# Kernel optimization log

Measured on AMD Instinct MI355X. Metric: run time of the kernel, lower is better.

Reference implementation:

```python
import jax, jax.numpy as jnp
import numpy as np

# AFD = permute -> VSSBlock (LN + SS2D Mamba selective scan, residual) -> permute
#       -> x + SAFM(ChannelLayerNorm(x))
C = 64        # in_channels (d_model)
DI = 128      # d_inner = expand(2) * d_model
N = 16        # d_state
R = 4         # dt_rank = ceil(64/16)
K = 4         # scan directions
LN_EPS = 1e-5
CN_EPS = 1e-6
B_, H_, W_ = 8, 64, 64


def setup_inputs() -> dict:
    key = jax.random.key(0)
    ks = jax.random.split(key, 16)
    f = lambda k, s, sc=0.02: jax.random.normal(k, s, jnp.float32) * sc
    return {
        'x': jax.random.normal(ks[0], (B_, C, H_, W_), jnp.float32),
        # VSSBlock ln_1
        'ln1_g': jnp.ones((C,), jnp.float32),
        'ln1_b': jnp.zeros((C,), jnp.float32),
        # SS2D
        'in_proj_w': f(ks[1], (2 * DI, C)),
        'in_proj_b': jnp.zeros((2 * DI,), jnp.float32),
        'conv_w': f(ks[2], (DI, 3, 3)),          # depthwise 3x3
        'conv_b': jnp.zeros((DI,), jnp.float32),
        'xproj_w': f(ks[3], (K, R + 2 * N, DI)),
        'dtproj_w': f(ks[4], (K, DI, R), 0.1),
        'dtproj_b': f(ks[5], (K, DI), 0.1),
        'A_logs': jnp.tile(jnp.log(jnp.arange(1, N + 1, dtype=jnp.float32)), (K * DI, 1)),
        'Ds': jnp.ones((K * DI,), jnp.float32),
        'outnorm_g': jnp.ones((DI,), jnp.float32),
        'outnorm_b': jnp.zeros((DI,), jnp.float32),
        'outproj_w': f(ks[6], (C, DI)),
        'outproj_b': jnp.zeros((C,), jnp.float32),
        # SAFM
        'mfr_w': f(ks[7], (4, C // 4, 3, 3)),    # 4 depthwise 3x3 convs
        'mfr_b': jnp.zeros((4, C // 4), jnp.float32),
        'aggr_w': f(ks[8], (C, C)),              # 1x1 conv
        'aggr_b': jnp.zeros((C,), jnp.float32),
        # channel LayerNorm (SAFMN-style, channels_first)
        'cn_g': jnp.ones((C,), jnp.float32),
        'cn_b': jnp.zeros((C,), jnp.float32),
    }


def _ln(x, g, b, eps):
    u = jnp.mean(x, -1, keepdims=True)
    v = jnp.mean((x - u) ** 2, -1, keepdims=True)
    return (x - u) * jax.lax.rsqrt(v + eps) * g + b


def _channel_ln(x, g, b):  # x: (B,C,H,W), normalize over C
    u = jnp.mean(x, 1, keepdims=True)
    v = jnp.mean((x - u) ** 2, 1, keepdims=True)
    return (x - u) * jax.lax.rsqrt(v + CN_EPS) * g[None, :, None, None] + b[None, :, None, None]


def _dwconv3(x, w, b):  # depthwise 3x3, pad 1. x: (B,C,H,W), w: (C,3,3)
    y = jax.lax.conv_general_dilated(x, w[:, None], (1, 1), 'SAME',
        dimension_numbers=('NCHW', 'OIHW', 'NCHW'), feature_group_count=x.shape[1])
    return y + b[None, :, None, None]


def _selective_scan(xs, dts, A, Bs, Cs, D):
    # xs,dts:(B,K,C,L)  Bs,Cs:(B,K,N,L)  A:(K,C,N)  D:(K,C)
    u = jnp.moveaxis(xs, -1, 0)
    dt = jnp.moveaxis(dts, -1, 0)
    Bl = jnp.moveaxis(Bs, -1, 0)
    Cl = jnp.moveaxis(Cs, -1, 0)

    def step(h, inp):
        u_t, dt_t, B_t, C_t = inp
        h = h * jnp.exp(dt_t[..., None] * A) + dt_t[..., None] * B_t[:, :, None, :] * u_t[..., None]
        return h, jnp.einsum('bkcn,bkn->bkc', h, C_t)

    h0 = jnp.zeros(u.shape[1:] + (A.shape[-1],), u.dtype)
    _, ys = jax.lax.scan(step, h0, (u, dt, Bl, Cl))
    return jnp.moveaxis(ys, 0, -1) + D[None, :, :, None] * xs


def _ss2d(x, in_proj_w, in_proj_b, conv_w, conv_b, xproj_w, dtproj_w, dtproj_b,
          A_logs, Ds, outnorm_g, outnorm_b, outproj_w, outproj_b):
    B, H, W, _ = x.shape
    L = H * W
    xz = jnp.einsum('bhwc,dc->bhwd', x, in_proj_w) + in_proj_b
    xi, z = jnp.split(xz, 2, axis=-1)
    xc = jnp.transpose(xi, (0, 3, 1, 2))                      # (B,DI,H,W)
    xc = jax.nn.silu(_dwconv3(xc, conv_w, conv_b))
    # 4-directional unfold: row-major, col-major, and their reverses
    x_flat = xc.reshape(B, DI, L)
    x_t = jnp.transpose(xc, (0, 1, 3, 2)).reshape(B, DI, L)
    x_hwwh = jnp.stack([x_flat, x_t], axis=1)                 # (B,2,DI,L)
    xs = jnp.concatenate([x_hwwh, jnp.flip(x_hwwh, axis=-1)], axis=1)  # (B,4,DI,L)
    x_dbl = jnp.einsum('bkdl,kcd->bkcl', xs, xproj_w)
    dts, Bs, Cs = jnp.split(x_dbl, [R, R + N], axis=2)
    dts = jnp.einsum('bkrl,kdr->bkdl', dts, dtproj_w)
    dts = jax.nn.softplus(dts + dtproj_b[None, :, :, None])
    A = -jnp.exp(A_logs).reshape(K, DI, N)
    out_y = _selective_scan(xs, dts, A, Bs, Cs, Ds.reshape(K, DI))  # (B,4,DI,L)
    inv = jnp.flip(out_y[:, 2:4], axis=-1)
    wh = jnp.transpose(out_y[:, 1].reshape(B, DI, W, H), (0, 1, 3, 2)).reshape(B, DI, L)
    invwh = jnp.transpose(inv[:, 1].reshape(B, DI, W, H), (0, 1, 3, 2)).reshape(B, DI, L)
    y = out_y[:, 0] + inv[:, 0] + wh + invwh                  # (B,DI,L)
    y = jnp.transpose(y, (0, 2, 1)).reshape(B, H, W, DI)
    y = _ln(y, outnorm_g, outnorm_b, LN_EPS) * jax.nn.silu(z)
    return jnp.einsum('bhwd,cd->bhwc', y, outproj_w) + outproj_b


def _safm(x, mfr_w, mfr_b, aggr_w, aggr_b):
    parts = jnp.split(x, 4, axis=1)
    outs = []
    for i in range(4):
        s = parts[i]
        k = 2 ** i
        if i > 0:  # adaptive max pool to (H/k, W/k) == maxpool k,k
            s = jax.lax.reduce_window(s, -jnp.inf, jax.lax.max, (1, 1, k, k), (1, 1, k, k), 'VALID')
        s = _dwconv3(s, mfr_w[i], mfr_b[i])
        if i > 0:  # nearest upsample back
            s = jnp.repeat(jnp.repeat(s, k, axis=2), k, axis=3)
        outs.append(s)
    out = jnp.concatenate(outs, axis=1)
    out = jnp.einsum('bchw,oc->bohw', out, aggr_w) + aggr_b[None, :, None, None]
    return jax.nn.gelu(out, approximate=False) * x


def reference(x, ln1_g, ln1_b, in_proj_w, in_proj_b, conv_w, conv_b, xproj_w,
              dtproj_w, dtproj_b, A_logs, Ds, outnorm_g, outnorm_b, outproj_w,
              outproj_b, mfr_w, mfr_b, aggr_w, aggr_b, cn_g, cn_b):
    xh = jnp.transpose(x, (0, 2, 3, 1))                       # NCHW -> NHWC
    xh = xh + _ss2d(_ln(xh, ln1_g, ln1_b, LN_EPS), in_proj_w, in_proj_b, conv_w,
                    conv_b, xproj_w, dtproj_w, dtproj_b, A_logs, Ds,
                    outnorm_g, outnorm_b, outproj_w, outproj_b)
    xo = jnp.transpose(xh, (0, 3, 1, 2))                      # NHWC -> NCHW
    return xo + _safm(_channel_ln(xo, cn_g, cn_b), mfr_w, mfr_b, aggr_w, aggr_b)
```

## Files before the change

kernel.cpp:

```cpp
#include <hip/hip_runtime.h>
#include <hip/hip_bf16.h>

#define BB 8
#define CC 64
#define HH 64
#define WW 64
#define LL 4096
#define DI 128
#define KK 4
#define NN 16
#define RR 4
#define XD 36
#define GG 64
#define TT 64

__device__ __forceinline__ float softplusf(float x){
    return fmaxf(x, 0.f) + __logf(1.f + __expf(-fabsf(x)));
}
__device__ __forceinline__ int p_of(int k, int t){
    int tt = (k & 2) ? (LL - 1 - t) : t;
    return (k & 1) ? ((tt & 63) * 64 + (tt >> 6)) : tt;
}

template<int CTRL>
__device__ __forceinline__ float dpp_xadd(float v){
    int t = __builtin_amdgcn_update_dpp(0, __float_as_int(v), CTRL, 0xF, 0xF, true);
    return v + __int_as_float(t);
}

__global__ __launch_bounds__(256) void k1_ln_inproj(
    const float* __restrict__ x,
    const float* __restrict__ ln1_g,
    const float* __restrict__ ln1_b,
    const float* __restrict__ ipw,
    const float* __restrict__ ipb,
    float* __restrict__ xi, float* __restrict__ zs)
{
    int bid = blockIdx.x;
    int b = bid >> 6, p0 = (bid & 63)*64;
    int tid = threadIdx.x;

    __shared__ float xs[64*65];
    __shared__ float lnxT[64*68];
    __shared__ float wT[16*260];
    __shared__ float gb[128];
    __shared__ float bias[256];
    __shared__ float red[512];
    __shared__ float mv[128];

    if (tid < 128) gb[tid] = (tid < 64) ? ln1_g[tid] : ln1_b[tid - 64];
    bias[tid] = ipb[tid];

    #pragma unroll
    for (int it = 0; it < 4; it++){
        int i = tid + it*256;
        int c = i >> 4, pq = i & 15;
        float4 v = *(const float4*)(x + ((size_t)(b*CC + c))*LL + p0 + pq*4);
        xs[(pq*4+0)*65 + c] = v.x;
        xs[(pq*4+1)*65 + c] = v.y;
        xs[(pq*4+2)*65 + c] = v.z;
        xs[(pq*4+3)*65 + c] = v.w;
    }
    __syncthreads();

    {
        int pix = tid >> 2, q = tid & 3;
        float s = 0.f, sq = 0.f;
        #pragma unroll
        for (int cc = 0; cc < 16; cc++){
            float v = xs[pix*65 + q*16 + cc];
            s += v; sq = fmaf(v, v, sq);
        }
        red[tid*2] = s; red[tid*2+1] = sq;
    }
    __syncthreads();
    if (tid < 64){
        float s = red[tid*8] + red[tid*8+2] + red[tid*8+4] + red[tid*8+6];
        float sq = red[tid*8+1] + red[tid*8+3] + red[tid*8+5] + red[tid*8+7];
        float mean = s * (1.f/64.f);
        float var  = sq * (1.f/64.f) - mean*mean;
        mv[tid*2] = mean; mv[tid*2+1] = rsqrtf(var + 1e-5f);
    }
    __syncthreads();
    {
        int pix = tid >> 2, q = tid & 3;
        float mean = mv[pix*2], rstd = mv[pix*2+1];
        #pragma unroll
        for (int cc = 0; cc < 16; cc++){
            int c = q*16 + cc;
            float v = (xs[pix*65 + c] - mean)*rstd*gb[c] + gb[64+c];
            lnxT[c*68 + pix] = v;
        }
    }

    int pt = tid >> 4, ot = tid & 15;
    float acc[16][4];
    #pragma unroll
    for (int j = 0; j < 16; j++)
        #pragma unroll
        for (int i2 = 0; i2 < 4; i2++) acc[j][i2] = 0.f;

    for (int kc = 0; kc < 4; kc++){
        __syncthreads();
        #pragma unroll
        for (int it = 0; it < 4; it++){
            int i = tid + it*256;
            int d = i >> 2, jq = i & 3;
            float4 wv = *(const float4*)(ipw + d*64 + kc*16 + jq*4);
            wT[(jq*4+0)*260 + d] = wv.x;
            wT[(jq*4+1)*260 + d] = wv.y;
            wT[(jq*4+2)*260 + d] = wv.z;
            wT[(jq*4+3)*260 + d] = wv.w;
        }
        __syncthreads();
        #pragma unroll
        for (int k = 0; k < 16; k++){
            float4 rv = *(const float4*)(lnxT + (kc*16 + k)*68 + pt*4);
            #pragma unroll
            for (int g = 0; g < 4; g++){
                float4 wv = *(const float4*)(wT + k*260 + g*64 + ot*4);
                acc[g*4+0][0] = fmaf(wv.x, rv.x, acc[g*4+0][0]);
                acc[g*4+0][1] = fmaf(wv.x, rv.y, acc[g*4+0][1]);
                acc[g*4+0][2] = fmaf(wv.x, rv.z, acc[g*4+0][2]);
                acc[g*4+0][3] = fmaf(wv.x, rv.w, acc[g*4+0][3]);
                acc[g*4+1][0] = fmaf(wv.y, rv.x, acc[g*4+1][0]);
                acc[g*4+1][1] = fmaf(wv.y, rv.y, acc[g*4+1][1]);
                acc[g*4+1][2] = fmaf(wv.y, rv.z, acc[g*4+1][2]);
                acc[g*4+1][3] = fmaf(wv.y, rv.w, acc[g*4+1][3]);
                acc[g*4+2][0] = fmaf(wv.z, rv.x, acc[g*4+2][0]);
                acc[g*4+2][1] = fmaf(wv.z, rv.y, acc[g*4+2][1]);
                acc[g*4+2][2] = fmaf(wv.z, rv.z, acc[g*4+2][2]);
                acc[g*4+2][3] = fmaf(wv.z, rv.w, acc[g*4+2][3]);
                acc[g*4+3][0] = fmaf(wv.w, rv.x, acc[g*4+3][0]);
                acc[g*4+3][1] = fmaf(wv.w, rv.y, acc[g*4+3][1]);
                acc[g*4+3][2] = fmaf(wv.w, rv.z, acc[g*4+3][2]);
                acc[g*4+3][3] = fmaf(wv.w, rv.w, acc[g*4+3][3]);
            }
        }
    }

    #pragma unroll
    for (int i2 = 0; i2 < 4; i2++){
        size_t prow = ((size_t)(b*LL) + p0 + pt*4 + i2);
        #pragma unroll
        for (int g = 0; g < 4; g++){
            int dbase = g*64 + ot*4;
            float4 v;
            v.x = acc[g*4+0][i2] + bias[dbase+0];
            v.y = acc[g*4+1][i2] + bias[dbase+1];
            v.z = acc[g*4+2][i2] + bias[dbase+2];
            v.w = acc[g*4+3][i2] + bias[dbase+3];
            if (g < 2){
                *(float4*)(xi + prow*DI + dbase) = v;
            } else {
                v.x = v.x / (1.f + __expf(-v.x));
                v.y = v.y / (1.f + __expf(-v.y));
                v.z = v.z / (1.f + __expf(-v.z));
                v.w = v.w / (1.f + __expf(-v.w));
                *(float4*)(zs + prow*DI + dbase - 128) = v;
            }
        }
    }
}

__global__ __launch_bounds__(256) void k2_dwconv(
    const float* __restrict__ xi,
    const float* __restrict__ cw,
    const float* __restrict__ cb,
    float* __restrict__ xc)
{
    int idx = blockIdx.x*256 + threadIdx.x;
    int d = idx & 127;
    int bp = idx >> 7;
    int p = bp & 4095, b = bp >> 12;
    int h = p >> 6, w = p & 63;
    float acc = cb[d];
    #pragma unroll
    for (int ky = 0; ky < 3; ky++){
        int hh = h + ky - 1;
        if ((unsigned)hh >= 64u) continue;
        #pragma unroll
        for (int kx = 0; kx < 3; kx++){
            int ww = w + kx - 1;
            if ((unsigned)ww >= 64u) continue;
            acc = fmaf(xi[((size_t)(b*LL) + hh*64 + ww)*DI + d], cw[d*9 + ky*3 + kx], acc);
        }
    }
    float sg = 1.f / (1.f + __expf(-acc));
    xc[idx] = acc * sg;
}

__global__ __launch_bounds__(256) void k3_xdbl(
    const float* __restrict__ xc,
    const float* __restrict__ xpw,
    float* __restrict__ xdbl)
{
    int bid = blockIdx.x;
    int b = bid >> 6, ptile = bid & 63;
    int tid = threadIdx.x;
    int ot = tid & 15;
    int pt = tid >> 4;

    __shared__ float r[64*132];
    __shared__ float wT[32*192];

    const float* xcb = xc + ((size_t)(b*LL) + ptile*64)*DI;
    for (int i = tid; i < 2048; i += 256){
        int pix = i >> 5, kq = i & 31;
        float4 v = *(const float4*)(xcb + pix*128 + kq*4);
        *(float4*)(r + pix*132 + kq*4) = v;
    }

    float acc[9][4];
    #pragma unroll
    for (int j = 0; j < 9; j++)
        #pragma unroll
        for (int i2 = 0; i2 < 4; i2++) acc[j][i2] = 0.f;

    for (int kc = 0; kc < 4; kc++){
        __syncthreads();
        int k0 = kc*32;
        for (int i = tid; i < 1152; i += 256){
            int cl = i >> 3, jq = i & 7;
            float4 wv = *(const float4*)(xpw + cl*128 + k0 + jq*4);
            int o = (cl*456) >> 12;
            int j = cl - o*9;
            wT[(jq*4+0)*192 + o*12 + j] = wv.x;
            wT[(jq*4+1)*192 + o*12 + j] = wv.y;
            wT[(jq*4+2)*192 + o*12 + j] = wv.z;
            wT[(jq*4+3)*192 + o*12 + j] = wv.w;
        }
        __syncthreads();
        const float* rbase = r + (pt*4)*132 + k0;
        #pragma unroll 4
        for (int k = 0; k < 32; k++){
            float4 wa = *(const float4*)(wT + k*192 + ot*12);
            float4 wb = *(const float4*)(wT + k*192 + ot*12 + 4);
            float w8 = wT[k*192 + ot*12 + 8];
            float rv0 = rbase[k];
            float rv1 = rbase[132 + k];
            float rv2 = rbase[264 + k];
            float rv3 = rbase[396 + k];
            float wv[9] = {wa.x, wa.y, wa.z, wa.w, wb.x, wb.y, wb.z, wb.w, w8};
            float rv[4] = {rv0, rv1, rv2, rv3};
            #pragma unroll
            for (int j = 0; j < 9; j++)
                #pragma unroll
                for (int i2 = 0; i2 < 4; i2++)
                    acc[j][i2] = fmaf(wv[j], rv[i2], acc[j][i2]);
        }
    }

    int kd = ot >> 2;
    int cbase = (ot & 3)*9;
    size_t obase = ((size_t)(b*KK + kd))*LL;
    #pragma unroll
    for (int i2 = 0; i2 < 4; i2++){
        int p = ptile*64 + pt*4 + i2;
        int tT = (p & 63)*64 + (p >> 6);
        int t = (kd == 0) ? p : (kd == 1) ? tT : (kd == 2) ? (4095 - p) : (4095 - tT);
        float* dst = xdbl + (obase + t)*XD + cbase;
        #pragma unroll
        for (int j = 0; j < 9; j++) dst[j] = acc[j][i2];
    }
}

__global__ __launch_bounds__(128, 4) void k4a_local(
    const float* __restrict__ xc, const float* __restrict__ xdbl,
    const float* __restrict__ dtw, const float* __restrict__ dtb,
    const float* __restrict__ A_logs,
    float* __restrict__ Pbuf, float* __restrict__ Hbuf)
{
    int bid = blockIdx.x;
    int cc = bid & 63, k = (bid >> 6) & 3, b = bid >> 8;
    int d = threadIdx.x;
    int kd = k*DI + d;
    float4 wv4 = *(const float4*)(dtw + kd*4);
    float bias = dtb[kd];
    float An[16];
    {
        const float4* al = (const float4*)(A_logs + kd*16);
        #pragma unroll
        for (int i = 0; i < 4; i++){
            float4 a = al[i];
            An[i*4+0] = -__expf(a.x); An[i*4+1] = -__expf(a.y);
            An[i*4+2] = -__expf(a.z); An[i*4+3] = -__expf(a.w);
        }
    }
    __shared__ float sraw[TT*XD];
    const float* src = xdbl + ((size_t)(b*KK + k)*LL + cc*TT)*XD;
    for (int i = threadIdx.x; i < TT*XD/4; i += 128)
        ((float4*)sraw)[i] = ((const float4*)src)[i];
    __syncthreads();

    const float* xcb = xc + (size_t)b*LL*DI;
    float h[16];
    #pragma unroll
    for (int i = 0; i < 16; i++) h[i] = 0.f;
    float Sdt = 0.f;
    for (int t = 0; t < TT; t++){
        const float* rp = sraw + t*XD;
        float4 xr = *(const float4*)rp;
        float dtr = fmaf(xr.x, wv4.x, fmaf(xr.y, wv4.y, fmaf(xr.z, wv4.z, fmaf(xr.w, wv4.w, bias))));
        float dt = softplusf(dtr);
        Sdt += dt;
        int p = p_of(k, cc*TT + t);
        float u = xcb[(size_t)p*DI + d];
        float du = dt * u;
        float4 B0 = *(const float4*)(rp + 4);
        float4 B1 = *(const float4*)(rp + 8);
        float4 B2 = *(const float4*)(rp + 12);
        float4 B3 = *(const float4*)(rp + 16);
        float Bv[16] = {B0.x,B0.y,B0.z,B0.w, B1.x,B1.y,B1.z,B1.w,
                        B2.x,B2.y,B2.z,B2.w, B3.x,B3.y,B3.z,B3.w};
        #pragma unroll
        for (int i = 0; i < 16; i++){
            float e = __expf(dt * An[i]);
            h[i] = fmaf(h[i], e, du * Bv[i]);
        }
    }
    size_t ob = ((size_t)bid)*2048 + d*16;
    #pragma unroll
    for (int i = 0; i < 16; i++){
        Pbuf[ob + i] = __expf(An[i] * Sdt);
        Hbuf[ob + i] = h[i];
    }
}

__global__ __launch_bounds__(256) void k4b_prop(
    const float* __restrict__ Pbuf, const float* __restrict__ Hbuf,
    float* __restrict__ hin_buf)
{
    int chain = blockIdx.x*256 + threadIdx.x;
    int bk = chain >> 11, s = chain & 2047;
    float hin = 0.f;
    for (int c = 0; c < GG; c++){
        size_t idx = ((size_t)(bk*GG + c))*2048 + s;
        hin_buf[idx] = hin;
        hin = fmaf(Pbuf[idx], hin, Hbuf[idx]);
    }
}

__global__ __launch_bounds__(128, 4) void k4c_emit(
    const float* __restrict__ xc, const float* __restrict__ xdbl,
    const float* __restrict__ dtw, const float* __restrict__ dtb,
    const float* __restrict__ A_logs, const float* __restrict__ Ds,
    const float* __restrict__ hin_buf,
    float* __restrict__ y)
{
    int bid = blockIdx.x;
    int cc = bid & 63, k = (bid >> 6) & 3, b = bid >> 8;
    int d = threadIdx.x;
    int kd = k*DI + d;
    float4 wv4 = *(const float4*)(dtw + kd*4);
    float bias = dtb[kd];
    float Dv = Ds[kd];
    float An[16];
    {
        const float4* al = (const float4*)(A_logs + kd*16);
        #pragma unroll
        for (int i = 0; i < 4; i++){
            float4 a = al[i];
            An[i*4+0] = -__expf(a.x); An[i*4+1] = -__expf(a.y);
            An[i*4+2] = -__expf(a.z); An[i*4+3] = -__expf(a.w);
        }
    }
    __shared__ float sraw[TT*XD];
    const float* src = xdbl + ((size_t)(b*KK + k)*LL + cc*TT)*XD;
    for (int i = threadIdx.x; i < TT*XD/4; i += 128)
        ((float4*)sraw)[i] = ((const float4*)src)[i];
    __syncthreads();

    const float* xcb = xc + (size_t)b*LL*DI;
    float* yb = y + (size_t)b*LL*DI;
    float h[16];
    {
        const float4* hi = (const float4*)(hin_buf + ((size_t)bid)*2048 + d*16);
        #pragma unroll
        for (int i = 0; i < 4; i++){
            float4 a = hi[i];
            h[i*4+0] = a.x; h[i*4+1] = a.y; h[i*4+2] = a.z; h[i*4+3] = a.w;
        }
    }
    for (int t = 0; t < TT; t++){
        const float* rp = sraw + t*XD;
        float4 xr = *(const float4*)rp;
        float dtr = fmaf(xr.x, wv4.x, fmaf(xr.y, wv4.y, fmaf(xr.z, wv4.z, fmaf(xr.w, wv4.w, bias))));
        float dt = softplusf(dtr);
        int p = p_of(k, cc*TT + t);
        float u = xcb[(size_t)p*DI + d];
        float du = dt * u;
        float4 B0 = *(const float4*)(rp + 4);
        float4 B1 = *(const float4*)(rp + 8);
        float4 B2 = *(const float4*)(rp + 12);
        float4 B3 = *(const float4*)(rp + 16);
        float Bv[16] = {B0.x,B0.y,B0.z,B0.w, B1.x,B1.y,B1.z,B1.w,
                        B2.x,B2.y,B2.z,B2.w, B3.x,B3.y,B3.z,B3.w};
        float4 C0 = *(const float4*)(rp + 20);
        float4 C1 = *(const float4*)(rp + 24);
        float4 C2 = *(const float4*)(rp + 28);
        float4 C3 = *(const float4*)(rp + 32);
        float Cv[16] = {C0.x,C0.y,C0.z,C0.w, C1.x,C1.y,C1.z,C1.w,
                        C2.x,C2.y,C2.z,C2.w, C3.x,C3.y,C3.z,C3.w};
        float yv = Dv * u;
        #pragma unroll
        for (int i = 0; i < 16; i++){
            float e = __expf(dt * An[i]);
            h[i] = fmaf(h[i], e, du * Bv[i]);
            yv = fmaf(h[i], Cv[i], yv);
        }
        atomicAdd(&yb[(size_t)p*DI + d], yv);
    }
}

__global__ __launch_bounds__(256) void k4_scan(
    const float* __restrict__ xc, const float* __restrict__ xdbl,
    const float* __restrict__ dtw, const float* __restrict__ dtb,
    const float* __restrict__ A_logs, const float* __restrict__ Ds,
    float* __restrict__ y)
{
    int bid = blockIdx.x;
    int b = bid >> 5, k = (bid >> 3) & 3, grp = bid & 7;
    int d0 = grp * 16;
    int tid = threadIdx.x;
    int wv = tid >> 6, lane = tid & 63, n = lane & 15, j = lane >> 4;
    int ch = wv*4 + j;
    int d = d0 + ch;
    int kd = k*DI + d;
    float An = -__expf(A_logs[kd*NN + n]);
    int ch_s = tid & 15;
    int kds = k*DI + d0 + ch_s;
    float w0s = dtw[kds*4+0], w1s = dtw[kds*4+1], w2s = dtw[kds*4+2], w3s = dtw[kds*4+3];
    float bs  = dtb[kds];
    float Dvs = Ds[kds];
    __shared__ float sraw[64*XD];
    __shared__ float sdd[64*16*2];
    __shared__ float sdy[64*17];
    const float* xdbase = xdbl + (size_t)(b*KK + k)*LL*XD;
    const float* xcb = xc + (size_t)b*LL*DI;
    float* yb = y + (size_t)b*LL*DI;
    float h = 0.f;
    for (int cc = 0; cc < 64; cc++){
        __syncthreads();
        const float* src = xdbase + (size_t)cc*64*XD;
        for (int i2 = tid; i2 < 576; i2 += 256)
            ((float4*)sraw)[i2] = ((const float4*)src)[i2];
        #pragma unroll
        for (int it = 0; it < 4; it++){
            int idx = tid + it*256;
            int t = idx >> 4;
            int pu = p_of(k, cc*64 + t);
            float u = xcb[(size_t)pu*DI + d0 + ch_s];
            float4 xr = *(const float4*)(src + t*XD);
            float dtr = fmaf(xr.x, w0s, fmaf(xr.y, w1s, fmaf(xr.z, w2s, fmaf(xr.w, w3s, bs))));
            float dt = softplusf(dtr);
            sdd[idx*2]     = dt;
            sdd[idx*2 + 1] = dt*u;
            sdy[t*17 + ch_s] = Dvs * u;
        }
        __syncthreads();
        #pragma unroll
        for (int tg = 0; tg < 4; tg++){
            float myv = 0.f;
            #pragma unroll
            for (int it = 0; it < 16; it++){
                int t = tg*16 + it;
                float dt = sdd[(t*16 + ch)*2];
                float du = sdd[(t*16 + ch)*2 + 1];
                float Bn = sraw[t*XD + 4 + n];
                float Cn = sraw[t*XD + 20 + n];
                float e = __expf(dt * An);
                h = fmaf(h, e, du * Bn);
                float yv = h * Cn;
                yv = dpp_xadd<0xB1>(yv);
                yv = dpp_xadd<0x4E>(yv);
                yv = dpp_xadd<0x141>(yv);
                yv = dpp_xadd<0x140>(yv);
                if (it == n) myv = yv;
            }
            int t = tg*16 + n;
            float yt = myv + sdy[t*17 + ch];
            int p = p_of(k, cc*64 + t);
            atomicAdd(&yb[(size_t)p*DI + d], yt);
        }
    }
}

__global__ __launch_bounds__(256) void k5_out(
    const float* __restrict__ y, const float* __restrict__ zs,
    const float* __restrict__ on_g, const float* __restrict__ on_b,
    const float* __restrict__ opw,
    const float* __restrict__ opb,
    const float* __restrict__ x,
    float* __restrict__ xo)
{
    int bid = blockIdx.x;
    int b = bid >> 6, p0 = (bid & 63)*64;
    int tid = threadIdx.x;

    __shared__ float vT[128*68];
    __shared__ float wT[128*68];
    __shared__ float gb[256];
    __shared__ float ob[64];
    __shared__ float red[512];
    __shared__ float mv[128];

    gb[tid] = (tid < 128) ? on_g[tid] : on_b[tid - 128];
    if (tid < 64) ob[tid] = opb[tid];

    #pragma unroll
    for (int it = 0; it < 8; it++){
        int i = tid + it*256;
        int c = i >> 5, jq = i & 31;
        float4 wv = *(const float4*)(opw + c*128 + jq*4);
        wT[(jq*4+0)*68 + c] = wv.x;
        wT[(jq*4+1)*68 + c] = wv.y;
        wT[(jq*4+2)*68 + c] = wv.z;
        wT[(jq*4+3)*68 + c] = wv.w;
    }

    int pix = tid >> 2, q = tid & 3;
    size_t base = ((size_t)(b*LL) + p0 + pix)*DI + q*32;
    float yv[32];
    {
        const float4* y4 = (const float4*)(y + base);
        float s = 0.f, sq = 0.f;
        #pragma unroll
        for (int i = 0; i < 8; i++){
            float4 a = y4[i];
            yv[i*4+0] = a.x; yv[i*4+1] = a.y; yv[i*4+2] = a.z; yv[i*4+3] = a.w;
            s += a.x + a.y + a.z + a.w;
            sq = fmaf(a.x,a.x, fmaf(a.y,a.y, fmaf(a.z,a.z, fmaf(a.w,a.w, sq))));
        }
        red[tid*2] = s; red[tid*2+1] = sq;
    }
    __syncthreads();
    if (tid < 64){
        float s = red[tid*8] + red[tid*8+2] + red[tid*8+4] + red[tid*8+6];
        float sq = red[tid*8+1] + red[tid*8+3] + red[tid*8+5] + red[tid*8+7];
        float mean = s * (1.f/128.f);
        float var  = sq * (1.f/128.f) - mean*mean;
        mv[tid*2] = mean; mv[tid*2+1] = rsqrtf(var + 1e-5f);
    }
    __syncthreads();
    {
        float mean = mv[pix*2], rstd = mv[pix*2+1];
        const float4* z4 = (const float4*)(zs + base);
        #pragma unroll
        for (int i = 0; i < 8; i++){
            float4 zz = z4[i];
            float zv[4] = {zz.x, zz.y, zz.z, zz.w};
            #pragma unroll
            for (int jj = 0; jj < 4; jj++){
                int d = q*32 + i*4 + jj;
                float vn = (yv[i*4+jj] - mean)*rstd*gb[d] + gb[128+d];
                vT[d*68 + pix] = vn * zv[jj];
            }
        }
    }
    __syncthreads();

    int pt = tid >> 4, ot = tid & 15;
    float acc[4][4];
    #pragma unroll
    for (int j = 0; j < 4; j++)
        #pragma unroll
        for (int i2 = 0; i2 < 4; i2++) acc[j][i2] = 0.f;

    #pragma unroll 4
    for (int k = 0; k < 128; k++){
        float4 rv = *(const float4*)(vT + k*68 + pt*4);
        float4 wv = *(const float4*)(wT + k*68 + ot*4);
        acc[0][0] = fmaf(wv.x, rv.x, acc[0][0]); acc[0][1] = fmaf(wv.x, rv.y, acc[0][1]);
        acc[0][2] = fmaf(wv.x, rv.z, acc[0][2]); acc[0][3] = fmaf(wv.x, rv.w, acc[0][3]);
        acc[1][0] = fmaf(wv.y, rv.x, acc[1][0]); acc[1][1] = fmaf(wv.y, rv.y, acc[1][1]);
        acc[1][2] = fmaf(wv.y, rv.z, acc[1][2]); acc[1][3] = fmaf(wv.y, rv.w, acc[1][3]);
        acc[2][0] = fmaf(wv.z, rv.x, acc[2][0]); acc[2][1] = fmaf(wv.z, rv.y, acc[2][1]);
        acc[2][2] = fmaf(wv.z, rv.z, acc[2][2]); acc[2][3] = fmaf(wv.z, rv.w, acc[2][3]);
        acc[3][0] = fmaf(wv.w, rv.x, acc[3][0]); acc[3][1] = fmaf(wv.w, rv.y, acc[3][1]);
        acc[3][2] = fmaf(wv.w, rv.z, acc[3][2]); acc[3][3] = fmaf(wv.w, rv.w, acc[3][3]);
    }

    #pragma unroll
    for (int jj = 0; jj < 4; jj++){
        int c = ot*4 + jj;
        float4 xr = *(const float4*)(x + ((size_t)(b*CC + c))*LL + p0 + pt*4);
        acc[jj][0] += ob[c] + xr.x;
        acc[jj][1] += ob[c] + xr.y;
        acc[jj][2] += ob[c] + xr.z;
        acc[jj][3] += ob[c] + xr.w;
    }
    #pragma unroll
    for (int i2 = 0; i2 < 4; i2++){
        float4 v = make_float4(acc[0][i2], acc[1][i2], acc[2][i2], acc[3][i2]);
        *(float4*)(xo + ((size_t)(b*LL) + p0 + pt*4 + i2)*CC + ot*4) = v;
    }
}

__global__ __launch_bounds__(256) void k6_chln(
    const float* __restrict__ xo,
    const float* __restrict__ cn_g, const float* __restrict__ cn_b,
    float* __restrict__ cl)
{
    int t = blockIdx.x*256 + threadIdx.x;
    int pix = t >> 2, q = t & 3;
    const float4* r4 = (const float4*)(xo + (size_t)pix*CC + q*16);
    float4 a[4];
    float s = 0.f, sq = 0.f;
    #pragma unroll
    for (int i = 0; i < 4; i++){
        a[i] = r4[i];
        s += a[i].x + a[i].y + a[i].z + a[i].w;
        sq = fmaf(a[i].x,a[i].x, fmaf(a[i].y,a[i].y, fmaf(a[i].z,a[i].z, fmaf(a[i].w,a[i].w, sq))));
    }
    s += __shfl_xor(s, 1, 64);  sq += __shfl_xor(sq, 1, 64);
    s += __shfl_xor(s, 2, 64);  sq += __shfl_xor(sq, 2, 64);
    float mean = s * (1.f/64.f);
    float var  = sq * (1.f/64.f) - mean*mean;
    float rstd = rsqrtf(var + 1e-6f);
    const float4* g4 = (const float4*)(cn_g + q*16);
    const float4* b4 = (const float4*)(cn_b + q*16);
    float4* o4 = (float4*)(cl + (size_t)pix*CC + q*16);
    #pragma unroll
    for (int i = 0; i < 4; i++){
        float4 g = g4[i], bb = b4[i], r;
        r.x = (a[i].x - mean)*rstd*g.x + bb.x;
        r.y = (a[i].y - mean)*rstd*g.y + bb.y;
        r.z = (a[i].z - mean)*rstd*g.z + bb.z;
        r.w = (a[i].w - mean)*rstd*g.w + bb.w;
        o4[i] = r;
    }
}

__global__ __launch_bounds__(256) void k7_pools(const float* __restrict__ cl, float* __restrict__ pools)
{
    int idx = blockIdx.x*256 + threadIdx.x;
    int g, S, base;
    if (idx < 131072)      { g = 1; S = 32; base = 0; }
    else if (idx < 163840) { g = 2; S = 16; base = 131072; idx -= 131072; }
    else if (idx < 172032) { g = 3; S = 8;  base = 163840; idx -= 163840; }
    else return;
    int pw = idx % S; idx /= S;
    int ph = idx % S; idx /= S;
    int j = idx & 15; int b = idx >> 4;
    int kk = 64 / S;
    int c = g*16 + j;
    float m = -1e30f;
    for (int dy = 0; dy < kk; dy++)
        for (int dx = 0; dx < kk; dx++){
            int h = ph*kk + dy, w = pw*kk + dx;
            m = fmaxf(m, cl[((size_t)(b*LL) + h*64 + w)*CC + c]);
        }
    pools[base + ((size_t)(b*16 + j)*S + ph)*S + pw] = m;
}

__global__ __launch_bounds__(256) void k8_mfr(
    const float* __restrict__ cl, const float* __restrict__ pools,
    const float* __restrict__ mfr_w,
    const float* __restrict__ mfr_b,
    float* __restrict__ cat)
{
    int idx = blockIdx.x*256 + threadIdx.x;
    int c = idx & 63; int bp = idx >> 6;
    int p = bp & 4095, b = bp >> 12;
    int g = c >> 4, j = c & 15;
    int h = p >> 6, w = p & 63;
    float acc = mfr_b[g*16 + j];
    const float* wr = mfr_w + (g*16 + j)*9;
    if (g == 0){
        #pragma unroll
        for (int ky = 0; ky < 3; ky++){
            int hh = h + ky - 1; if ((unsigned)hh >= 64u) continue;
            #pragma unroll
            for (int kx = 0; kx < 3; kx++){
                int ww = w + kx - 1; if ((unsigned)ww >= 64u) continue;
                acc = fmaf(cl[((size_t)(b*LL) + hh*64 + ww)*CC + c], wr[ky*3 + kx], acc);
            }
        }
    } else {
        int S = 64 >> g;
        int ph = h >> g, pw = w >> g;
        int base = (g == 1) ? 0 : ((g == 2) ? 131072 : 163840);
        const float* P = pools + base + (size_t)(b*16 + j)*S*S;
        #pragma unroll
        for (int ky = 0; ky < 3; ky++){
            int hh = ph + ky - 1; if ((unsigned)hh >= (unsigned)S) continue;
            #pragma unroll
            for (int kx = 0; kx < 3; kx++){
                int ww = pw + kx - 1; if ((unsigned)ww >= (unsigned)S) continue;
                acc = fmaf(P[hh*S + ww], wr[ky*3 + kx], acc);
            }
        }
    }
    cat[idx] = acc;
}

__global__ __launch_bounds__(256) void k9_agg(
    const float* __restrict__ cat, const float* __restrict__ cl, const float* __restrict__ xo,
    const float* __restrict__ agw,
    const float* __restrict__ agb,
    float* __restrict__ out)
{
    int bid = blockIdx.x;
    int b = bid >> 6, p0 = (bid & 63)*64;
    int tid = threadIdx.x;

    __shared__ float catT[64*68];
    __shared__ float wT[64*68];
    __shared__ float ab[64];

    if (tid < 64) ab[tid] = agb[tid];
    #pragma unroll
    for (int it = 0; it < 4; it++){
        int i = tid + it*256;
        int pix = i >> 4, cq = i & 15;
        float4 v = *(const float4*)(cat + ((size_t)(b*LL) + p0 + pix)*CC + cq*4);
        catT[(cq*4+0)*68 + pix] = v.x;
        catT[(cq*4+1)*68 + pix] = v.y;
        catT[(cq*4+2)*68 + pix] = v.z;
        catT[(cq*4+3)*68 + pix] = v.w;
        int o = i >> 4;
        float4 wv = *(const float4*)(agw + o*64 + cq*4);
        wT[(cq*4+0)*68 + o] = wv.x;
        wT[(cq*4+1)*68 + o] = wv.y;
        wT[(cq*4+2)*68 + o] = wv.z;
        wT[(cq*4+3)*68 + o] = wv.w;
    }
    __syncthreads();

    int pt = tid >> 4, ot = tid & 15;
    float acc[4][4];
    #pragma unroll
    for (int j = 0; j < 4; j++)
        #pragma unroll
        for (int i2 = 0; i2 < 4; i2++) acc[j][i2] = 0.f;

    #pragma unroll 4
    for (int k = 0; k < 64; k++){
        float4 rv = *(const float4*)(catT + k*68 + pt*4);
        float4 wv = *(const float4*)(wT + k*68 + ot*4);
        acc[0][0] = fmaf(wv.x, rv.x, acc[0][0]); acc[0][1] = fmaf(wv.x, rv.y, acc[0][1]);
        acc[0][2] = fmaf(wv.x, rv.z, acc[0][2]); acc[0][3] = fmaf(wv.x, rv.w, acc[0][3]);
        acc[1][0] = fmaf(wv.y, rv.x, acc[1][0]); acc[1][1] = fmaf(wv.y, rv.y, acc[1][1]);
        acc[1][2] = fmaf(wv.y, rv.z, acc[1][2]); acc[1][3] = fmaf(wv.y, rv.w, acc[1][3]);
        acc[2][0] = fmaf(wv.z, rv.x, acc[2][0]); acc[2][1] = fmaf(wv.z, rv.y, acc[2][1]);
        acc[2][2] = fmaf(wv.z, rv.z, acc[2][2]); acc[2][3] = fmaf(wv.z, rv.w, acc[2][3]);
        acc[3][0] = fmaf(wv.w, rv.x, acc[3][0]); acc[3][1] = fmaf(wv.w, rv.y, acc[3][1]);
        acc[3][2] = fmaf(wv.w, rv.z, acc[3][2]); acc[3][3] = fmaf(wv.w, rv.w, acc[3][3]);
    }

    float res[4][4];
    #pragma unroll
    for (int i2 = 0; i2 < 4; i2++){
        size_t prow = ((size_t)(b*LL) + p0 + pt*4 + i2)*CC + ot*4;
        float4 clv = *(const float4*)(cl + prow);
        float4 xov = *(const float4*)(xo + prow);
        float cla[4] = {clv.x, clv.y, clv.z, clv.w};
        float xoa[4] = {xov.x, xov.y, xov.z, xov.w};
        #pragma unroll
        for (int jj = 0; jj < 4; jj++){
            float av = acc[jj][i2] + ab[ot*4 + jj];
            float gl = 0.5f*av*(1.f + erff(av*0.70710678118f));
            res[jj][i2] = xoa[jj] + gl*cla[jj];
        }
    }
    #pragma unroll
    for (int jj = 0; jj < 4; jj++){
        int o = ot*4 + jj;
        float4 v = make_float4(res[jj][0], res[jj][1], res[jj][2], res[jj][3]);
        *(float4*)(out + ((size_t)(b*CC + o))*LL + p0 + pt*4) = v;
    }
}

extern "C" void kernel_launch(void* const* d_in, const int* in_sizes, int n_in,
                              void* d_out, int out_size, void* d_ws, size_t ws_size,
                              hipStream_t stream)
{
    const float* x       = (const float*)d_in[0];
    const float* ln1_g   = (const float*)d_in[1];
    const float* ln1_b   = (const float*)d_in[2];
    const float* ipw     = (const float*)d_in[3];
    const float* ipb     = (const float*)d_in[4];
    const float* conv_w  = (const float*)d_in[5];
    const float* conv_b  = (const float*)d_in[6];
    const float* xpw     = (const float*)d_in[7];
    const float* dtw     = (const float*)d_in[8];
    const float* dtb     = (const float*)d_in[9];
    const float* A_logs  = (const float*)d_in[10];
    const float* Ds      = (const float*)d_in[11];
    const float* on_g    = (const float*)d_in[12];
    const float* on_b    = (const float*)d_in[13];
    const float* opw     = (const float*)d_in[14];
    const float* opb     = (const float*)d_in[15];
    const float* mfr_w   = (const float*)d_in[16];
    const float* mfr_b   = (const float*)d_in[17];
    const float* agw     = (const float*)d_in[18];
    const float* agb     = (const float*)d_in[19];
    const float* cn_g    = (const float*)d_in[20];
    const float* cn_b    = (const float*)d_in[21];
    float* out = (float*)d_out;

    float* ws = (float*)d_ws;
    float* xi    = ws;
    float* zs    = ws + 4194304;
    float* xc    = ws + 8388608;
    float* xdbl  = ws + 12582912;
    float* y     = xi;
    float* xo    = xc;
    float* pools = xc + 2097152;
    float* cl    = xdbl;
    float* cat   = zs;
    float* Pbuf  = ws + 17301504;
    float* Hbuf  = ws + 21495808;
    float* hinb  = ws + 25690112;
    bool par = ws_size >= (size_t)29884416 * 4;

    hipLaunchKernelGGL(k1_ln_inproj, dim3(BB*64), dim3(256), 0, stream,
                       x, ln1_g, ln1_b, ipw, ipb, xi, zs);
    hipLaunchKernelGGL(k2_dwconv, dim3(BB*LL*DI/256), dim3(256), 0, stream,
                       xi, conv_w, conv_b, xc);
    hipLaunchKernelGGL(k3_xdbl, dim3(BB*64), dim3(256), 0, stream,
                       xc, xpw, xdbl);
    hipMemsetAsync(y, 0, (size_t)BB*LL*DI*sizeof(float), stream);
    if (par){
        hipLaunchKernelGGL(k4a_local, dim3(BB*KK*GG), dim3(128), 0, stream,
                           xc, xdbl, dtw, dtb, A_logs, Pbuf, Hbuf);
        hipLaunchKernelGGL(k4b_prop, dim3(256), dim3(256), 0, stream,
                           Pbuf, Hbuf, hinb);
        hipLaunchKernelGGL(k4c_emit, dim3(BB*KK*GG), dim3(128), 0, stream,
                           xc, xdbl, dtw, dtb, A_logs, Ds, hinb, y);
    } else {
        hipLaunchKernelGGL(k4_scan, dim3(256), dim3(256), 0, stream,
                           xc, xdbl, dtw, dtb, A_logs, Ds, y);
    }
    hipLaunchKernelGGL(k5_out, dim3(BB*64), dim3(256), 0, stream,
                       y, zs, on_g, on_b, opw, opb, x, xo);
    hipLaunchKernelGGL(k6_chln, dim3(BB*LL*4/256), dim3(256), 0, stream,
                       xo, cn_g, cn_b, cl);
    hipLaunchKernelGGL(k7_pools, dim3((172032 + 255)/256), dim3(256), 0, stream,
                       cl, pools);
    hipLaunchKernelGGL(k8_mfr, dim3(BB*LL*CC/256), dim3(256), 0, stream,
                       cl, pools, mfr_w, mfr_b, cat);
    hipLaunchKernelGGL(k9_agg, dim3(BB*64), dim3(256), 0, stream,
                       cat, cl, xo, agw, agb, out);
}
```

Measured before the change: 423.5 us.

## Split scan states across thread pairs, register-block dwconv, fuse channel LN into out-proj

The depthwise conv now computes four adjacent pixels per thread, reusing loaded row values and hoisting the weights into registers. The chunked scan kernels split the 16 states of each channel across two threads and use exp2 with pre-scaled A values. In the emit kernel the two halves are combined with a DPP lane-pair add before a single atomic. The channel LayerNorm is folded into the output-projection kernel through a shared-memory reduction, which removes one launch and one full read and write of the activation. Together these aim to raise parallelism in the latency-bound scan and cut memory traffic, at the cost of more threads per block, extra barriers and more shared memory in k5.

```diff
diff --git a/kernel.cpp b/kernel.cpp
--- a/kernel.cpp
+++ b/kernel.cpp
@@ -171,23 +171,38 @@
 {
     int idx = blockIdx.x*256 + threadIdx.x;
     int d = idx & 127;
-    int bp = idx >> 7;
-    int p = bp & 4095, b = bp >> 12;
-    int h = p >> 6, w = p & 63;
-    float acc = cb[d];
+    int g = idx >> 7;
+    int p0 = (g & 1023) * 4;
+    int b = g >> 10;
+    int h = p0 >> 6, w0 = p0 & 63;
+    float wt[9];
+    #pragma unroll
+    for (int j = 0; j < 9; j++) wt[j] = cw[d*9 + j];
+    float bv = cb[d];
+    float acc[4] = {bv, bv, bv, bv};
     #pragma unroll
     for (int ky = 0; ky < 3; ky++){
         int hh = h + ky - 1;
         if ((unsigned)hh >= 64u) continue;
-        #pragma unroll
-        for (int kx = 0; kx < 3; kx++){
-            int ww = w + kx - 1;
-            if ((unsigned)ww >= 64u) continue;
-            acc = fmaf(xi[((size_t)(b*LL) + hh*64 + ww)*DI + d], cw[d*9 + ky*3 + kx], acc);
-        }
-    }
-    float sg = 1.f / (1.f + __expf(-acc));
-    xc[idx] = acc * sg;
+        const float* row = xi + ((size_t)(b*LL) + hh*64)*DI + d;
+        float v0 = (w0 > 0)  ? row[(w0-1)*DI] : 0.f;
+        float v1 = row[(w0+0)*DI];
+        float v2 = row[(w0+1)*DI];
+        float v3 = row[(w0+2)*DI];
+        float v4 = row[(w0+3)*DI];
+        float v5 = (w0 < 60) ? row[(w0+4)*DI] : 0.f;
+        float wa = wt[ky*3], wbv = wt[ky*3+1], wc = wt[ky*3+2];
+        acc[0] = fmaf(v0, wa, fmaf(v1, wbv, fmaf(v2, wc, acc[0])));
+        acc[1] = fmaf(v1, wa, fmaf(v2, wbv, fmaf(v3, wc, acc[1])));
+        acc[2] = fmaf(v2, wa, fmaf(v3, wbv, fmaf(v4, wc, acc[2])));
+        acc[3] = fmaf(v3, wa, fmaf(v4, wbv, fmaf(v5, wc, acc[3])));
+    }
+    #pragma unroll
+    for (int i = 0; i < 4; i++){
+        float a = acc[i];
+        float sg = 1.f / (1.f + __expf(-a));
+        xc[((size_t)(b*LL) + p0 + i)*DI + d] = a * sg;
+    }
 }
 
 __global__ __launch_bounds__(256) void k3_xdbl(
@@ -265,7 +280,7 @@
     }
 }
 
-__global__ __launch_bounds__(128, 4) void k4a_local(
+__global__ __launch_bounds__(256, 8) void k4a_local(
     const float* __restrict__ xc, const float* __restrict__ xdbl,
     const float* __restrict__ dtw, const float* __restrict__ dtb,
     const float* __restrict__ A_logs,
@@ -273,30 +288,33 @@
 {
     int bid = blockIdx.x;
     int cc = bid & 63, k = (bid >> 6) & 3, b = bid >> 8;
-    int d = threadIdx.x;
+    int tid = threadIdx.x;
+    int d = tid >> 1, half = tid & 1;
     int kd = k*DI + d;
     float4 wv4 = *(const float4*)(dtw + kd*4);
     float bias = dtb[kd];
-    float An[16];
+    float An2[8];
     {
-        const float4* al = (const float4*)(A_logs + kd*16);
-        #pragma unroll
-        for (int i = 0; i < 4; i++){
+        const float4* al = (const float4*)(A_logs + kd*16 + half*8);
+        #pragma unroll
+        for (int i = 0; i < 2; i++){
             float4 a = al[i];
-            An[i*4+0] = -__expf(a.x); An[i*4+1] = -__expf(a.y);
-            An[i*4+2] = -__expf(a.z); An[i*4+3] = -__expf(a.w);
+            An2[i*4+0] = -__expf(a.x) * 1.44269504f;
+            An2[i*4+1] = -__expf(a.y) * 1.44269504f;
+            An2[i*4+2] = -__expf(a.z) * 1.44269504f;
+            An2[i*4+3] = -__expf(a.w) * 1.44269504f;
         }
     }
     __shared__ float sraw[TT*XD];
     const float* src = xdbl + ((size_t)(b*KK + k)*LL + cc*TT)*XD;
-    for (int i = threadIdx.x; i < TT*XD/4; i += 128)
+    for (int i = tid; i < TT*XD/4; i += 256)
         ((float4*)sraw)[i] = ((const float4*)src)[i];
     __syncthreads();
 
     const float* xcb = xc + (size_t)b*LL*DI;
-    float h[16];
-    #pragma unroll
-    for (int i = 0; i < 16; i++) h[i] = 0.f;
+    float h[8];
+    #pragma unroll
+    for (int i = 0; i < 8; i++) h[i] = 0.f;
     float Sdt = 0.f;
     for (int t = 0; t < TT; t++){
         const float* rp = sraw + t*XD;
@@ -307,22 +325,21 @@
         int p = p_of(k, cc*TT + t);
         float u = xcb[(size_t)p*DI + d];
         float du = dt * u;
-        float4 B0 = *(const float4*)(rp + 4);
-        float4 B1 = *(const float4*)(rp + 8);
-        float4 B2 = *(const float4*)(rp + 12);
-        float4 B3 = *(const float4*)(rp + 16);
-        float Bv[16] = {B0.x,B0.y,B0.z,B0.w, B1.x,B1.y,B1.z,B1.w,
-                        B2.x,B2.y,B2.z,B2.w, B3.x,B3.y,B3.z,B3.w};
-        #pragma unroll
-        for (int i = 0; i < 16; i++){
-            float e = __expf(dt * An[i]);
-            h[i] = fmaf(h[i], e, du * Bv[i]);
-        }
-    }
-    size_t ob = ((size_t)bid)*2048 + d*16;
-    #pragma unroll
-    for (int i = 0; i < 16; i++){
-        Pbuf[ob + i] = __expf(An[i] * Sdt);
+        float4 B0 = *(const float4*)(rp + 4 + half*8);
+        float4 B1 = *(const float4*)(rp + 8 + half*8);
+        h[0] = fmaf(h[0], exp2f(dt*An2[0]), du*B0.x);
+        h[1] = fmaf(h[1], exp2f(dt*An2[1]), du*B0.y);
+        h[2] = fmaf(h[2], exp2f(dt*An2[2]), du*B0.z);
+        h[3] = fmaf(h[3], exp2f(dt*An2[3]), du*B0.w);
+        h[4] = fmaf(h[4], exp2f(dt*An2[4]), du*B1.x);
+        h[5] = fmaf(h[5], exp2f(dt*An2[5]), du*B1.y);
+        h[6] = fmaf(h[6], exp2f(dt*An2[6]), du*B1.z);
+        h[7] = fmaf(h[7], exp2f(dt*An2[7]), du*B1.w);
+    }
+    size_t ob = ((size_t)bid)*2048 + d*16 + half*8;
+    #pragma unroll
+    for (int i = 0; i < 8; i++){
+        Pbuf[ob + i] = exp2f(An2[i] * Sdt);
         Hbuf[ob + i] = h[i];
     }
 }
@@ -341,7 +358,7 @@
     }
 }
 
-__global__ __launch_bounds__(128, 4) void k4c_emit(
+__global__ __launch_bounds__(256, 6) void k4c_emit(
     const float* __restrict__ xc, const float* __restrict__ xdbl,
     const float* __restrict__ dtw, const float* __restrict__ dtb,
     const float* __restrict__ A_logs, const float* __restrict__ Ds,
@@ -350,37 +367,38 @@
 {
     int bid = blockIdx.x;
     int cc = bid & 63, k = (bid >> 6) & 3, b = bid >> 8;
-    int d = threadIdx.x;
+    int tid = threadIdx.x;
+    int d = tid >> 1, half = tid & 1;
     int kd = k*DI + d;
     float4 wv4 = *(const float4*)(dtw + kd*4);
     float bias = dtb[kd];
     float Dv = Ds[kd];
-    float An[16];
+    float An2[8];
     {
-        const float4* al = (const float4*)(A_logs + kd*16);
-        #pragma unroll
-        for (int i = 0; i < 4; i++){
+        const float4* al = (const float4*)(A_logs + kd*16 + half*8);
+        #pragma unroll
+        for (int i = 0; i < 2; i++){
             float4 a = al[i];
-            An[i*4+0] = -__expf(a.x); An[i*4+1] = -__expf(a.y);
-            An[i*4+2] = -__expf(a.z); An[i*4+3] = -__expf(a.w);
+            An2[i*4+0] = -__expf(a.x) * 1.44269504f;
+            An2[i*4+1] = -__expf(a.y) * 1.44269504f;
+            An2[i*4+2] = -__expf(a.z) * 1.44269504f;
+            An2[i*4+3] = -__expf(a.w) * 1.44269504f;
         }
     }
     __shared__ float sraw[TT*XD];
     const float* src = xdbl + ((size_t)(b*KK + k)*LL + cc*TT)*XD;
-    for (int i = threadIdx.x; i < TT*XD/4; i += 128)
+    for (int i = tid; i < TT*XD/4; i += 256)
         ((float4*)sraw)[i] = ((const float4*)src)[i];
     __syncthreads();
 
     const float* xcb = xc + (size_t)b*LL*DI;
     float* yb = y + (size_t)b*LL*DI;
-    float h[16];
+    float h[8];
     {
-        const float4* hi = (const float4*)(hin_buf + ((size_t)bid)*2048 + d*16);
-        #pragma unroll
-        for (int i = 0; i < 4; i++){
-            float4 a = hi[i];
-            h[i*4+0] = a.x; h[i*4+1] = a.y; h[i*4+2] = a.z; h[i*4+3] = a.w;
-        }
+        const float4* hi = (const float4*)(hin_buf + ((size_t)bid)*2048 + d*16 + half*8);
+        float4 a0 = hi[0], a1 = hi[1];
+        h[0]=a0.x; h[1]=a0.y; h[2]=a0.z; h[3]=a0.w;
+        h[4]=a1.x; h[5]=a1.y; h[6]=a1.z; h[7]=a1.w;
     }
     for (int t = 0; t < TT; t++){
         const float* rp = sraw + t*XD;
@@ -390,26 +408,22 @@
         int p = p_of(k, cc*TT + t);
         float u = xcb[(size_t)p*DI + d];
         float du = dt * u;
-        float4 B0 = *(const float4*)(rp + 4);
-        float4 B1 = *(const float4*)(rp + 8);
-        float4 B2 = *(const float4*)(rp + 12);
-        float4 B3 = *(const float4*)(rp + 16);
-        float Bv[16] = {B0.x,B0.y,B0.z,B0.w, B1.x,B1.y,B1.z,B1.w,
-                        B2.x,B2.y,B2.z,B2.w, B3.x,B3.y,B3.z,B3.w};
-        float4 C0 = *(const float4*)(rp + 20);
-        float4 C1 = *(const float4*)(rp + 24);
-        float4 C2 = *(const float4*)(rp + 28);
-        float4 C3 = *(const float4*)(rp + 32);
-        float Cv[16] = {C0.x,C0.y,C0.z,C0.w, C1.x,C1.y,C1.z,C1.w,
-                        C2.x,C2.y,C2.z,C2.w, C3.x,C3.y,C3.z,C3.w};
-        float yv = Dv * u;
-        #pragma unroll
-        for (int i = 0; i < 16; i++){
-            float e = __expf(dt * An[i]);
-            h[i] = fmaf(h[i], e, du * Bv[i]);
-            yv = fmaf(h[i], Cv[i], yv);
-        }
-        atomicAdd(&yb[(size_t)p*DI + d], yv);
+        float4 B0 = *(const float4*)(rp + 4 + half*8);
+        float4 B1 = *(const float4*)(rp + 8 + half*8);
+        float4 C0 = *(const float4*)(rp + 20 + half*8);
+        float4 C1 = *(const float4*)(rp + 24 + half*8);
+        float yv = half ? 0.f : Dv * u;
+        h[0] = fmaf(h[0], exp2f(dt*An2[0]), du*B0.x); yv = fmaf(h[0], C0.x, yv);
+        h[1] = fmaf(h[1], exp2f(dt*An2[1]), du*B0.y); yv = fmaf(h[1], C0.y, yv);
+        h[2] = fmaf(h[2], exp2f(dt*An2[2]), du*B0.z); yv = fmaf(h[2], C0.z, yv);
+        h[3] = fmaf(h[3], exp2f(dt*An2[3]), du*B0.w); yv = fmaf(h[3], C0.w, yv);
+        h[4] = fmaf(h[4], exp2f(dt*An2[4]), du*B1.x); yv = fmaf(h[4], C1.x, yv);
+        h[5] = fmaf(h[5], exp2f(dt*An2[5]), du*B1.y); yv = fmaf(h[5], C1.y, yv);
+        h[6] = fmaf(h[6], exp2f(dt*An2[6]), du*B1.z); yv = fmaf(h[6], C1.z, yv);
+        h[7] = fmaf(h[7], exp2f(dt*An2[7]), du*B1.w); yv = fmaf(h[7], C1.w, yv);
+        yv = dpp_xadd<0xB1>(yv);
+        if (half == 0)
+            atomicAdd(&yb[(size_t)p*DI + d], yv);
     }
 }
 
@@ -492,7 +506,8 @@
     const float* __restrict__ opw,
     const float* __restrict__ opb,
     const float* __restrict__ x,
-    float* __restrict__ xo)
+    const float* __restrict__ cn_g, const float* __restrict__ cn_b,
+    float* __restrict__ xo, float* __restrict__ cl)
 {
     int bid = blockIdx.x;
     int b = bid >> 6, p0 = (bid & 63)*64;
@@ -502,11 +517,13 @@
     __shared__ float wT[128*68];
     __shared__ float gb[256];
     __shared__ float ob[64];
-    __shared__ float red[512];
+    __shared__ float cgb[128];
+    __shared__ float red[2048];
     __shared__ float mv[128];
 
     gb[tid] = (tid < 128) ? on_g[tid] : on_b[tid - 128];
     if (tid < 64) ob[tid] = opb[tid];
+    if (tid >= 128 && tid < 256) cgb[tid-128] = (tid < 192) ? cn_g[tid-128] : cn_b[tid-192];
 
     #pragma unroll
     for (int it = 0; it < 8; it++){
@@ -552,9 +569,9 @@
             float zv[4] = {zz.x, zz.y, zz.z, zz.w};
             #pragma unroll
             for (int jj = 0; jj < 4; jj++){
-                int d = q*32 + i*4 + jj;
-                float vn = (yv[i*4+jj] - mean)*rstd*gb[d] + gb[128+d];
-                vT[d*68 + pix] = vn * zv[jj];
+                int dd = q*32 + i*4 + jj;
+                float vn = (yv[i*4+jj] - mean)*rstd*gb[dd] + gb[128+dd];
+                vT[dd*68 + pix] = vn * zv[jj];
             }
         }
     }
@@ -595,40 +612,38 @@
         float4 v = make_float4(acc[0][i2], acc[1][i2], acc[2][i2], acc[3][i2]);
         *(float4*)(xo + ((size_t)(b*LL) + p0 + pt*4 + i2)*CC + ot*4) = v;
     }
-}
-
-__global__ __launch_bounds__(256) void k6_chln(
-    const float* __restrict__ xo,
-    const float* __restrict__ cn_g, const float* __restrict__ cn_b,
-    float* __restrict__ cl)
-{
-    int t = blockIdx.x*256 + threadIdx.x;
-    int pix = t >> 2, q = t & 3;
-    const float4* r4 = (const float4*)(xo + (size_t)pix*CC + q*16);
-    float4 a[4];
-    float s = 0.f, sq = 0.f;
-    #pragma unroll
-    for (int i = 0; i < 4; i++){
-        a[i] = r4[i];
-        s += a[i].x + a[i].y + a[i].z + a[i].w;
-        sq = fmaf(a[i].x,a[i].x, fmaf(a[i].y,a[i].y, fmaf(a[i].z,a[i].z, fmaf(a[i].w,a[i].w, sq))));
-    }
-    s += __shfl_xor(s, 1, 64);  sq += __shfl_xor(sq, 1, 64);
-    s += __shfl_xor(s, 2, 64);  sq += __shfl_xor(sq, 2, 64);
-    float mean = s * (1.f/64.f);
-    float var  = sq * (1.f/64.f) - mean*mean;
-    float rstd = rsqrtf(var + 1e-6f);
-    const float4* g4 = (const float4*)(cn_g + q*16);
-    const float4* b4 = (const float4*)(cn_b + q*16);
-    float4* o4 = (float4*)(cl + (size_t)pix*CC + q*16);
-    #pragma unroll
-    for (int i = 0; i < 4; i++){
-        float4 g = g4[i], bb = b4[i], r;
-        r.x = (a[i].x - mean)*rstd*g.x + bb.x;
-        r.y = (a[i].y - mean)*rstd*g.y + bb.y;
-        r.z = (a[i].z - mean)*rstd*g.z + bb.z;
-        r.w = (a[i].w - mean)*rstd*g.w + bb.w;
-        o4[i] = r;
+
+    __syncthreads();
+    #pragma unroll
+    for (int i2 = 0; i2 < 4; i2++){
+        float s = acc[0][i2] + acc[1][i2] + acc[2][i2] + acc[3][i2];
+        float sq = fmaf(acc[0][i2],acc[0][i2], fmaf(acc[1][i2],acc[1][i2],
+                   fmaf(acc[2][i2],acc[2][i2], acc[3][i2]*acc[3][i2])));
+        red[(pt*4 + i2)*16 + ot] = s;
+        red[1024 + (pt*4 + i2)*16 + ot] = sq;
+    }
+    __syncthreads();
+    if (tid < 64){
+        float s = 0.f, sq = 0.f;
+        #pragma unroll
+        for (int o = 0; o < 16; o++){
+            s += red[tid*16 + o];
+            sq += red[1024 + tid*16 + o];
+        }
+        float mean = s * (1.f/64.f);
+        float var  = sq * (1.f/64.f) - mean*mean;
+        mv[tid*2] = mean; mv[tid*2+1] = rsqrtf(var + 1e-6f);
+    }
+    __syncthreads();
+    #pragma unroll
+    for (int i2 = 0; i2 < 4; i2++){
+        float mean = mv[(pt*4+i2)*2], rstd = mv[(pt*4+i2)*2+1];
+        float4 v;
+        v.x = (acc[0][i2] - mean)*rstd*cgb[ot*4+0] + cgb[64+ot*4+0];
+        v.y = (acc[1][i2] - mean)*rstd*cgb[ot*4+1] + cgb[64+ot*4+1];
+        v.z = (acc[2][i2] - mean)*rstd*cgb[ot*4+2] + cgb[64+ot*4+2];
+        v.w = (acc[3][i2] - mean)*rstd*cgb[ot*4+3] + cgb[64+ot*4+3];
+        *(float4*)(cl + ((size_t)(b*LL) + p0 + pt*4 + i2)*CC + ot*4) = v;
     }
 }
 
@@ -817,26 +832,24 @@
 
     hipLaunchKernelGGL(k1_ln_inproj, dim3(BB*64), dim3(256), 0, stream,
                        x, ln1_g, ln1_b, ipw, ipb, xi, zs);
-    hipLaunchKernelGGL(k2_dwconv, dim3(BB*LL*DI/256), dim3(256), 0, stream,
+    hipLaunchKernelGGL(k2_dwconv, dim3(BB*LL*DI/1024), dim3(256), 0, stream,
                        xi, conv_w, conv_b, xc);
     hipLaunchKernelGGL(k3_xdbl, dim3(BB*64), dim3(256), 0, stream,
                        xc, xpw, xdbl);
     hipMemsetAsync(y, 0, (size_t)BB*LL*DI*sizeof(float), stream);
     if (par){
-        hipLaunchKernelGGL(k4a_local, dim3(BB*KK*GG), dim3(128), 0, stream,
+        hipLaunchKernelGGL(k4a_local, dim3(BB*KK*GG), dim3(256), 0, stream,
                            xc, xdbl, dtw, dtb, A_logs, Pbuf, Hbuf);
         hipLaunchKernelGGL(k4b_prop, dim3(256), dim3(256), 0, stream,
                            Pbuf, Hbuf, hinb);
-        hipLaunchKernelGGL(k4c_emit, dim3(BB*KK*GG), dim3(128), 0, stream,
+        hipLaunchKernelGGL(k4c_emit, dim3(BB*KK*GG), dim3(256), 0, stream,
                            xc, xdbl, dtw, dtb, A_logs, Ds, hinb, y);
     } else {
         hipLaunchKernelGGL(k4_scan, dim3(256), dim3(256), 0, stream,
                            xc, xdbl, dtw, dtb, A_logs, Ds, y);
     }
     hipLaunchKernelGGL(k5_out, dim3(BB*64), dim3(256), 0, stream,
-                       y, zs, on_g, on_b, opw, opb, x, xo);
-    hipLaunchKernelGGL(k6_chln, dim3(BB*LL*4/256), dim3(256), 0, stream,
-                       xo, cn_g, cn_b, cl);
+                       y, zs, on_g, on_b, opw, opb, x, cn_g, cn_b, xo, cl);
     hipLaunchKernelGGL(k7_pools, dim3((172032 + 255)/256), dim3(256), 0, stream,
                        cl, pools);
     hipLaunchKernelGGL(k8_mfr, dim3(BB*LL*CC/256), dim3(256), 0, stream,
```

Measured after the change: 449.8 us. 6.2% more time.
